# Performance work log

Measured on AMD Instinct MI355X. Metric: run time of the kernel, lower is better.

Reference implementation:

```python
import jax, jax.numpy as jnp
import numpy as np

N_NODES = 10000
DIM = 512
HEADS = 8
HEAD_DIM = DIM // HEADS  # 64
TOPK = 6
EPS = 1e-5
SLOPE = 0.01  # torch LeakyReLU default


def _layernorm(x, w, b):
    mu = x.mean(axis=-1, keepdims=True)
    var = ((x - mu) ** 2).mean(axis=-1, keepdims=True)
    return (x - mu) / jnp.sqrt(var + EPS) * w + b


def setup_inputs() -> dict:
    key = jax.random.key(0)
    ks = jax.random.split(key, 8)

    def w(k, shape):
        return jax.random.normal(k, shape, dtype=jnp.float32) * 0.02

    return {
        "x": jax.random.normal(ks[0], (1, N_NODES, DIM), dtype=jnp.float32),
        "fc1_w": w(ks[1], (DIM, DIM)), "fc1_b": jnp.zeros((DIM,), jnp.float32),
        "wh_w": w(ks[2], (DIM, DIM)), "wh_b": jnp.zeros((DIM,), jnp.float32),
        "wt_w": w(ks[3], (DIM, DIM)), "wt_b": jnp.zeros((DIM,), jnp.float32),
        "q_w": w(ks[4], (DIM, DIM)), "q_b": jnp.zeros((DIM,), jnp.float32),
        "kv_w": w(ks[5], (2 * DIM, DIM)), "kv_b": jnp.zeros((2 * DIM,), jnp.float32),
        "lin_w": w(ks[6], (DIM, DIM)), "lin_b": jnp.zeros((DIM,), jnp.float32),
        "norm_w": jnp.ones((DIM,), jnp.float32),
        "norm_b": jnp.zeros((DIM,), jnp.float32),
    }


def reference(x, fc1_w, fc1_b, wh_w, wh_b, wt_w, wt_b, q_w, q_b,
              kv_w, kv_b, lin_w, lin_b, norm_w, norm_b):
    # x: [1, N, DIM]
    n = x.shape[1]
    scale = HEAD_DIM ** -0.5

    x_input = x
    h = jax.nn.leaky_relu(x @ fc1_w.T + fc1_b, SLOPE)
    h = (h + h.mean(axis=1, keepdims=True)) * 0.5

    e_h = h @ wh_w.T + wh_b            # [1, N, DIM]
    e_t = h @ wt_w.T + wt_b            # [1, N, DIM]

    # dense graph-construction scores + per-row top-k neighbors
    logits = (e_h * scale) @ jnp.swapaxes(e_t, -2, -1)   # [1, N, N]
    _, topk_idx = jax.lax.top_k(logits, TOPK)            # [1, N, TOPK]

    # prototype node = most frequent tail index (torch unique+counts+argsort, top=1)
    counts = jnp.bincount(topk_idx.reshape(-1), length=n)
    top_node = jnp.argmax(counts)

    ins_top = jnp.take(x_input, top_node[None], axis=1)  # [1, 1, DIM]
    q_feat = jnp.take(h, top_node[None], axis=1)[0, 0]   # [DIM]

    # gather k=TOPK neighbor tail embeddings per node
    nb = e_t[0][topk_idx[0]]                              # [N, TOPK, DIM]

    q_heads = (q_feat @ q_w.T + q_b).reshape(HEADS, HEAD_DIM) * scale
    kv = (nb @ kv_w.T + kv_b).reshape(n, TOPK, 2, HEADS, HEAD_DIM)
    k_, v_ = kv[:, :, 0], kv[:, :, 1]                     # [N, TOPK, H, HD]

    attn = jnp.einsum('hd,nehd->nhe', q_heads, k_)        # [N, H, TOPK]
    attn = jax.nn.softmax(attn, axis=-1)
    out = jnp.einsum('nhe,nehd->nhd', attn, v_).reshape(n, DIM)

    e_nh = _layernorm(out, norm_w, norm_b)[None]          # [1, N, DIM]

    s = _layernorm(e_h + e_nh, norm_w, norm_b)
    s = jax.nn.leaky_relu(s @ lin_w.T + lin_b, SLOPE)     # dropout = identity (eval)
    embedding = s + x_input
    return embedding, ins_top
```

## Files before the change

### kernel.cpp

```cpp
#include <hip/hip_runtime.h>
#include <hip/hip_bf16.h>
#include <math.h>

#define N_NODES 10000
#define DIM 512
#define TOPK 6
#define NCHUNK 10
#define CHUNK 1024
#define NL 4
#define NCK 8
#define NC2 16
#define SLOPE 0.01
#define LN_EPS 1e-5f

typedef short bf16x8 __attribute__((ext_vector_type(8)));
typedef float f32x4 __attribute__((ext_vector_type(4)));
typedef double f64x4 __attribute__((ext_vector_type(4)));

__device__ __forceinline__ unsigned pack_key(float v, int idx)
{
    unsigned b = __float_as_uint(v);
    unsigned m = b ^ ((unsigned)((int)b >> 31) | 0x80000000u);
    return (m & 0xFFFFC000u) | (16383u - (unsigned)idx);
}

template <int D>
__device__ __forceinline__ void insert_u(unsigned (&k)[D], unsigned nk)
{
    if (nk > k[D - 1]) {
        k[D - 1] = nk;
#pragma unroll
        for (int s = D - 1; s > 0; s--) {
            unsigned hi = max(k[s], k[s - 1]);
            unsigned lo = min(k[s], k[s - 1]);
            k[s - 1] = hi; k[s] = lo;
        }
    }
}

__device__ __forceinline__ void gload16(const void* g, void* l)
{
    __builtin_amdgcn_global_load_lds(
        (const __attribute__((address_space(1))) void*)g,
        (__attribute__((address_space(3))) void*)l, 16, 0, 0);
}

__global__ __launch_bounds__(256) void colsum_part64(
    const double* __restrict__ h, double* __restrict__ part, int n, int nb)
{
    int b = blockIdx.x;
    int rows_per = (n + nb - 1) / nb;
    int r0 = b * rows_per, r1 = min(n, r0 + rows_per);
    int t = threadIdx.x;
    double s0 = 0.0, s1 = 0.0;
    for (int i = r0; i < r1; i++) {
        s0 += h[(size_t)i * DIM + t];
        s1 += h[(size_t)i * DIM + t + 256];
    }
    part[b * DIM + t] = s0;
    part[b * DIM + t + 256] = s1;
}

__global__ void colmean64(const double* __restrict__ part, double* __restrict__ mean,
                          int nb, int n)
{
    int j = blockIdx.x * blockDim.x + threadIdx.x;
    if (j < DIM) {
        double s = 0.0;
        for (int b = 0; b < nb; b++) s += part[b * DIM + j];
        mean[j] = s / (double)n;
    }
}

__global__ void cast_eh(const double* __restrict__ in, float* __restrict__ of,
                        short* __restrict__ ob)
{
    int i = (blockIdx.x * blockDim.x + threadIdx.x) * 4;
    double2 v0 = *(const double2*)(in + i);
    double2 v1 = *(const double2*)(in + i + 2);
    float4 f = make_float4((float)v0.x, (float)v0.y, (float)v1.x, (float)v1.y);
    *(float4*)(of + i) = f;
    __hip_bfloat16 b0 = __float2bfloat16(f.x), b1 = __float2bfloat16(f.y);
    __hip_bfloat16 b2 = __float2bfloat16(f.z), b3 = __float2bfloat16(f.w);
    short4 s = make_short4(*(short*)&b0, *(short*)&b1, *(short*)&b2, *(short*)&b3);
    *(short4*)(ob + i) = s;
}

__global__ void cast_et(const double* __restrict__ in, short* __restrict__ ob)
{
    int i = (blockIdx.x * blockDim.x + threadIdx.x) * 4;
    double2 v0 = *(const double2*)(in + i);
    double2 v1 = *(const double2*)(in + i + 2);
    __hip_bfloat16 b0 = __float2bfloat16((float)v0.x), b1 = __float2bfloat16((float)v0.y);
    __hip_bfloat16 b2 = __float2bfloat16((float)v1.x), b3 = __float2bfloat16((float)v1.y);
    short4 s = make_short4(*(short*)&b0, *(short*)&b1, *(short*)&b2, *(short*)&b3);
    *(short4*)(ob + i) = s;
}

__global__ void cast_wb(const float* __restrict__ in1, short* __restrict__ o1, int n1,
                        const float* __restrict__ in2, short* __restrict__ o2)
{
    int i = (blockIdx.x * blockDim.x + threadIdx.x) * 4;
    const float* in = (i < n1) ? in1 + i : in2 + (i - n1);
    short* o = (i < n1) ? o1 + i : o2 + (i - n1);
    float4 f = *(const float4*)in;
    __hip_bfloat16 b0 = __float2bfloat16(f.x), b1 = __float2bfloat16(f.y);
    __hip_bfloat16 b2 = __float2bfloat16(f.z), b3 = __float2bfloat16(f.w);
    *(short4*)o = make_short4(*(short*)&b0, *(short*)&b1, *(short*)&b2, *(short*)&b3);
}

template <int POST, bool AF32, bool MIX>
__global__ __launch_bounds__(256, 4) void mfma_gemm_f64(
    const void* __restrict__ Av, const float* __restrict__ W,
    const float* __restrict__ bias, const double* __restrict__ mn,
    double* __restrict__ C, int n, int K, int M)
{
    __shared__ double As[64][18];
    __shared__ double Bs[128][18];
    const int t = threadIdx.x, lane = t & 63, wid = t >> 6;
    const int lx = lane & 15, q = lane >> 4;
    const int wr = (wid >> 1) * 32, wc = (wid & 1) * 64;
    const int i0 = blockIdx.x * 64, j0 = blockIdx.y * 128;

    f64x4 acc[2][4];
#pragma unroll
    for (int a = 0; a < 2; a++)
#pragma unroll
        for (int b = 0; b < 4; b++) acc[a][b] = (f64x4)0.0;

    const int arow = t >> 2, askq = (t & 3) * 4;
    int gi = i0 + arow; if (gi >= n) gi = n - 1;
    const float*  af32 = (const float*)Av + (size_t)gi * K + askq;
    const double* af64 = (const double*)Av + (size_t)gi * K + askq;
    const int brow = t >> 1, bskq = (t & 1) * 8;
    const float* wrow = W + (size_t)(j0 + brow) * K + bskq;

    float4 wv0 = *(const float4*)(wrow);
    float4 wv1 = *(const float4*)(wrow + 4);
    float4 av;
    double2 a0v, a1v;
    if (AF32) av = *(const float4*)(af32);
    else { a0v = *(const double2*)(af64); a1v = *(const double2*)(af64 + 2); }

    for (int k0 = 0; k0 < K; k0 += 16) {
        __syncthreads();
        double m0 = 0, m1 = 0, m2 = 0, m3 = 0;
        if (MIX) {
            double2 mv0 = *(const double2*)(mn + k0 + askq);
            double2 mv1 = *(const double2*)(mn + k0 + askq + 2);
            m0 = mv0.x; m1 = mv0.y; m2 = mv1.x; m3 = mv1.y;
        }
        if (AF32) {
            As[arow][askq]     = (double)av.x; As[arow][askq + 1] = (double)av.y;
            As[arow][askq + 2] = (double)av.z; As[arow][askq + 3] = (double)av.w;
        } else if (MIX) {
            As[arow][askq]     = (a0v.x + m0) * 0.5; As[arow][askq + 1] = (a0v.y + m1) * 0.5;
            As[arow][askq + 2] = (a1v.x + m2) * 0.5; As[arow][askq + 3] = (a1v.y + m3) * 0.5;
        } else {
            As[arow][askq]     = a0v.x; As[arow][askq + 1] = a0v.y;
            As[arow][askq + 2] = a1v.x; As[arow][askq + 3] = a1v.y;
        }
        Bs[brow][bskq]     = (double)wv0.x; Bs[brow][bskq + 1] = (double)wv0.y;
        Bs[brow][bskq + 2] = (double)wv0.z; Bs[brow][bskq + 3] = (double)wv0.w;
        Bs[brow][bskq + 4] = (double)wv1.x; Bs[brow][bskq + 5] = (double)wv1.y;
        Bs[brow][bskq + 6] = (double)wv1.z; Bs[brow][bskq + 7] = (double)wv1.w;
        if (k0 + 16 < K) {
            wv0 = *(const float4*)(wrow + k0 + 16);
            wv1 = *(const float4*)(wrow + k0 + 20);
            if (AF32) av = *(const float4*)(af32 + k0 + 16);
            else { a0v = *(const double2*)(af64 + k0 + 16);
                   a1v = *(const double2*)(af64 + k0 + 18); }
        }
        __syncthreads();

#pragma unroll
        for (int ks = 0; ks < 4; ks++) {
            double a0 = As[wr + lx][ks * 4 + q];
            double a1 = As[wr + 16 + lx][ks * 4 + q];
#pragma unroll
            for (int cf = 0; cf < 4; cf++) {
                double b = Bs[wc + cf * 16 + lx][ks * 4 + q];
                acc[0][cf] = __builtin_amdgcn_mfma_f64_16x16x4f64(a0, b, acc[0][cf], 0, 0, 0);
                acc[1][cf] = __builtin_amdgcn_mfma_f64_16x16x4f64(a1, b, acc[1][cf], 0, 0, 0);
            }
        }
    }

#pragma unroll
    for (int rf = 0; rf < 2; rf++)
#pragma unroll
        for (int cf = 0; cf < 4; cf++)
#pragma unroll
            for (int reg = 0; reg < 4; reg++) {
                int gi2 = i0 + wr + rf * 16 + q * 4 + reg;
                int gj2 = j0 + wc + cf * 16 + lx;
                if (gi2 < n) {
                    double v = acc[rf][cf][reg] + (double)bias[gj2];
                    if (POST == 1) v = (v >= 0.0) ? v : v * SLOPE;
                    C[(size_t)gi2 * M + gj2] = v;
                }
            }
}

__global__ __launch_bounds__(256, 3) void logits_topk_mfma(
    const short* __restrict__ eh, const short* __restrict__ et,
    unsigned* __restrict__ pk, int n)
{
    __shared__ short As[3 * 4096];
    __shared__ short Bs[3 * 4096];
    const int t = threadIdx.x;
    const int lane = t & 63, wid = t >> 6;
    const int lx = lane & 15, q = lane >> 4;

    int id = blockIdx.x, bx, chunk;
    if (id < 632) { chunk = id & 7; bx = id >> 3; }
    else { int r = id - 632; chunk = 8 + (r & 1); bx = r >> 1; }
    const int i0 = bx * 128;
    const int wbase = wid * 32;

    const int jlo = chunk * CHUNK;
    const int jhi = min(n, jlo + CHUNK);
    const int nj = (jhi - jlo + 127) >> 7;
    const int np = nj * 16;

    const int sslot = (t & 3) ^ ((t >> 3) & 3);
    const short* aP[2];
    const short* bP[2];
#pragma unroll
    for (int is = 0; is < 2; is++) {
        int row = is * 64 + (t >> 2);
        int ra = i0 + row; if (ra >= n) ra = n - 1;
        aP[is] = eh + (size_t)ra * DIM + sslot * 8;
    }
    const int slotq = (q ^ ((lx >> 1) & 3)) * 8;
    const int aOff = (wbase + lx) * 32 + slotq;
    const int bOff = lx * 32 + slotq;

    unsigned keys[8][NL];
#pragma unroll
    for (int r = 0; r < 8; r++)
#pragma unroll
        for (int s = 0; s < NL; s++) keys[r][s] = 0u;

    f32x4 acc[2][8];
#pragma unroll
    for (int rf = 0; rf < 2; rf++)
#pragma unroll
        for (int cf = 0; cf < 8; cf++) acc[rf][cf] = (f32x4)0.f;

    auto STAGE = [&](int buf, int ph) {
        int kk = ph & 15;
        if (kk == 0) {
            int j0 = jlo + (ph >> 4) * 128;
#pragma unroll
            for (int is = 0; is < 2; is++) {
                int row = is * 64 + (t >> 2);
                int rb = j0 + row; if (rb >= n) rb = n - 1;
                bP[is] = et + (size_t)rb * DIM + sslot * 8;
            }
        }
        int ko = kk * 32;
#pragma unroll
        for (int is = 0; is < 2; is++) {
            gload16(aP[is] + ko, &As[buf * 4096 + is * 2048 + wid * 512]);
            gload16(bP[is] + ko, &Bs[buf * 4096 + is * 2048 + wid * 512]);
        }
    };

    STAGE(0, 0);
    STAGE(1, 1);
    int cb = 0;
    for (int p = 0; p < np; ++p) {
        __builtin_amdgcn_sched_barrier(0);
        __builtin_amdgcn_s_barrier();
        __builtin_amdgcn_sched_barrier(0);
        if (p + 2 < np) {
            int nb = cb + 2; if (nb >= 3) nb -= 3;
            STAGE(nb, p + 2);
            asm volatile("s_waitcnt vmcnt(8)" ::: "memory");
        } else if (p + 1 < np) {
            asm volatile("s_waitcnt vmcnt(4)" ::: "memory");
        } else {
            asm volatile("s_waitcnt vmcnt(0)" ::: "memory");
        }
        __builtin_amdgcn_sched_barrier(0);
        __builtin_amdgcn_s_barrier();
        __builtin_amdgcn_sched_barrier(0);

        const short* Ab = As + cb * 4096;
        const short* Bb = Bs + cb * 4096;
        bf16x8 a0 = *(const bf16x8*)(Ab + aOff);
        bf16x8 a1 = *(const bf16x8*)(Ab + aOff + 512);
#pragma unroll
        for (int cf = 0; cf < 8; cf++) {
            bf16x8 bw = *(const bf16x8*)(Bb + bOff + cf * 512);
            acc[0][cf] = __builtin_amdgcn_mfma_f32_16x16x32_bf16(
                a0, bw, acc[0][cf], 0, 0, 0);
            acc[1][cf] = __builtin_amdgcn_mfma_f32_16x16x32_bf16(
                a1, bw, acc[1][cf], 0, 0, 0);
        }

        if ((p & 15) == 15) {
            int j0 = jlo + (p >> 4) * 128;
#pragma unroll
            for (int rf = 0; rf < 2; rf++)
#pragma unroll
                for (int cf = 0; cf < 8; cf++) {
                    int gj = j0 + cf * 16 + lx;
                    if (gj < n) {
#pragma unroll
                        for (int reg = 0; reg < 4; reg++)
                            insert_u<NL>(keys[rf * 4 + reg],
                                         pack_key(acc[rf][cf][reg], gj));
                    }
                    acc[rf][cf] = (f32x4)0.f;
                }
        }
        cb = (cb == 2) ? 0 : cb + 1;
    }

#pragma unroll
    for (int rr = 0; rr < 8; rr++) {
        unsigned mk[NCK];
#pragma unroll
        for (int s = 0; s < NL; s++) mk[s] = keys[rr][s];
#pragma unroll
        for (int s = NL; s < NCK; s++) mk[s] = 0u;
        for (int m = 1; m < 16; m <<= 1) {
            unsigned sv[NCK];
#pragma unroll
            for (int s = 0; s < NCK; s++) sv[s] = mk[s];
#pragma unroll
            for (int s = 0; s < NCK; s++) {
                unsigned ov = (unsigned)__shfl_xor((int)sv[s], m);
                insert_u<NCK>(mk, ov);
            }
        }
        if (lx == 0) {
            int rf = rr >> 2, reg = rr & 3;
            int grow = i0 + wbase + rf * 16 + q * 4 + reg;
            if (grow < n) {
#pragma unroll
                for (int s = 0; s < NCK; s++)
                    pk[((size_t)chunk * N_NODES + grow) * NCK + s] = mk[s];
            }
        }
    }
}

template <int POST>
__global__ __launch_bounds__(256, 3) void mfma_gemm_bf16(
    const short* __restrict__ A, const short* __restrict__ W,
    const float* __restrict__ bias, const float* __restrict__ res,
    float* __restrict__ C, int n, int M)
{
    __shared__ short As[2][8192];
    __shared__ short Bs[2][8192];
    const int t = threadIdx.x;
    const int lane = t & 63, wid = t >> 6;
    const int lx = lane & 15, q = lane >> 4;
    const int lx7 = lane & 7;
    const int i0 = blockIdx.x * 128;
    const int j0 = blockIdx.y * 128;
    const int wbase = wid * 32;
    const int srl = lane >> 3;
    const int swz = (lane & 7) ^ srl;

    const short* aP[4];
    const short* bP[4];
#pragma unroll
    for (int is = 0; is < 4; is++) {
        int ra = i0 + is * 32 + wid * 8 + srl; if (ra >= n) ra = n - 1;
        aP[is] = A + (size_t)ra * DIM + swz * 8;
        int rb = j0 + is * 32 + wid * 8 + srl;
        bP[is] = W + (size_t)rb * DIM + swz * 8;
    }
    int aIdx[2], bIdx[2];
#pragma unroll
    for (int ks = 0; ks < 2; ks++) {
        int kap = (ks * 4 + q) ^ lx7;
        aIdx[ks] = (wbase + lx) * 64 + kap * 8;
        bIdx[ks] = lx * 64 + kap * 8;
    }

    f32x4 acc[2][8];
#pragma unroll
    for (int rf = 0; rf < 2; rf++)
#pragma unroll
        for (int cf = 0; cf < 8; cf++) acc[rf][cf] = (f32x4)0.f;

    auto STAGE = [&](int buf, int kk) {
        int ko = kk * 64;
        short* ab = &As[buf][wid * 512];
        short* bb = &Bs[buf][wid * 512];
#pragma unroll
        for (int is = 0; is < 4; is++) {
            gload16(aP[is] + ko, ab + is * 2048);
            gload16(bP[is] + ko, bb + is * 2048);
        }
    };

    STAGE(0, 0);
    for (int p = 0; p < 8; ++p) {
        __builtin_amdgcn_sched_barrier(0);
        __builtin_amdgcn_s_barrier();
        __builtin_amdgcn_sched_barrier(0);
        if (p + 1 < 8) {
            STAGE((p + 1) & 1, p + 1);
            asm volatile("s_waitcnt vmcnt(8)" ::: "memory");
        } else {
            asm volatile("s_waitcnt vmcnt(0)" ::: "memory");
        }
        __builtin_amdgcn_sched_barrier(0);
        __builtin_amdgcn_s_barrier();
        __builtin_amdgcn_sched_barrier(0);

        const short* Ab = As[p & 1];
        const short* Bb = Bs[p & 1];
#pragma unroll
        for (int ks = 0; ks < 2; ks++) {
            bf16x8 a0 = *(const bf16x8*)(Ab + aIdx[ks]);
            bf16x8 a1 = *(const bf16x8*)(Ab + aIdx[ks] + 1024);
#pragma unroll
            for (int cf = 0; cf < 8; cf++) {
                bf16x8 bw = *(const bf16x8*)(Bb + bIdx[ks] + cf * 1024);
                acc[0][cf] = __builtin_amdgcn_mfma_f32_16x16x32_bf16(
                    a0, bw, acc[0][cf], 0, 0, 0);
                acc[1][cf] = __builtin_amdgcn_mfma_f32_16x16x32_bf16(
                    a1, bw, acc[1][cf], 0, 0, 0);
            }
        }
    }

#pragma unroll
    for (int rf = 0; rf < 2; rf++)
#pragma unroll
        for (int cf = 0; cf < 8; cf++)
#pragma unroll
            for (int reg = 0; reg < 4; reg++) {
                int gi = i0 + wbase + rf * 16 + q * 4 + reg;
                int gj = j0 + cf * 16 + lx;
                if (gi < n) {
                    float v = acc[rf][cf][reg] + bias[gj];
                    if (POST >= 1) v = (v >= 0.f) ? v : v * SLOPE;
                    if (POST == 2) v += res[(size_t)gi * M + gj];
                    C[(size_t)gi * M + gj] = v;
                }
            }
}

__global__ void merge_chunks16(const unsigned* __restrict__ pk,
                               int* __restrict__ cand, int n)
{
    int row = blockIdx.x * blockDim.x + threadIdx.x;
    if (row >= n) return;
    unsigned bk[NC2];
#pragma unroll
    for (int s = 0; s < NC2; s++) bk[s] = 0u;
    for (int c = 0; c < NCHUNK; c++) {
#pragma unroll
        for (int s = 0; s < NCK; s++)
            insert_u<NC2>(bk, pk[((size_t)c * n + row) * NCK + s]);
    }
#pragma unroll
    for (int s = 0; s < NC2; s++)
        cand[row * NC2 + s] = 16383 - (int)(bk[s] & 16383u);
}

__global__ __launch_bounds__(64) void refine16(
    const double* __restrict__ ehd, const double* __restrict__ etd,
    const int* __restrict__ cand, int* __restrict__ tki,
    int* __restrict__ counts, int n)
{
    int row = blockIdx.x;
    int lane = threadIdx.x;
    int c = lane >> 2, sub = lane & 3;
    int j = cand[row * NC2 + c];
    const double* er = ehd + (size_t)row * DIM;
    const double* tr = etd + (size_t)j * DIM;
    double s = 0.0;
#pragma unroll 8
    for (int k = sub; k < DIM; k += 4) s += er[k] * tr[k];
    s += __shfl_down(s, 2);
    s += __shfl_down(s, 1);
    double mine = __shfl(s, lane & ~3);
    int rank = 0;
#pragma unroll
    for (int m = 0; m < NC2; m++) {
        double vm = __shfl(s, m * 4);
        int jm = __shfl(j, m * 4);
        bool better = (vm > mine) || (vm == mine && jm < j);
        rank += better ? 1 : 0;
    }
    if (sub == 0 && rank < TOPK) {
        tki[row * TOPK + rank] = j;
        atomicAdd(&counts[j], 1);
    }
}

__global__ __launch_bounds__(1024) void argmax_kernel(
    const int* __restrict__ counts, int n, const float* __restrict__ x,
    int* __restrict__ topn, float* __restrict__ out_ins)
{
    __shared__ unsigned long long red[1024];
    int t = threadIdx.x;
    unsigned long long best = 0;
    for (int j = t; j < n; j += 1024) {
        unsigned long long key =
            ((unsigned long long)(unsigned)counts[j] << 32) | (unsigned)(n - 1 - j);
        if (key > best) best = key;
    }
    red[t] = best;
    __syncthreads();
    for (int s = 512; s > 0; s >>= 1) {
        if (t < s && red[t + s] > red[t]) red[t] = red[t + s];
        __syncthreads();
    }
    int tn = n - 1 - (int)(red[0] & 0xffffffffu);
    if (t == 0) *topn = tn;
    if (t < DIM) out_ins[t] = x[(size_t)tn * DIM + t];
}

__global__ __launch_bounds__(512) void qheads_kernel(
    const double* __restrict__ h2d, const double* __restrict__ mn,
    const int* __restrict__ topn, const float* __restrict__ qw,
    const float* __restrict__ qb, float* __restrict__ qh)
{
    __shared__ float qf[DIM];
    int t = threadIdx.x;
    int tn = *topn;
    qf[t] = (float)((h2d[(size_t)tn * DIM + t] + mn[t]) * 0.5);
    __syncthreads();
    int w = t >> 6, lane = t & 63;
    int jrow = blockIdx.x * 8 + w;
    float s = 0.f;
    for (int k = lane; k < DIM; k += 64) s += qf[k] * qw[(size_t)jrow * DIM + k];
#pragma unroll
    for (int m = 32; m > 0; m >>= 1) s += __shfl_down(s, m);
    if (lane == 0) qh[jrow] = (s + qb[jrow]) * 0.125f;
}

__global__ __launch_bounds__(512) void scores_kernel(
    const float* __restrict__ E, const float* __restrict__ qh, float* __restrict__ sc)
{
    int i = blockIdx.x;
    int t = threadIdx.x, w = t >> 6, lane = t & 63;
    float v = qh[t] * E[(size_t)i * 1024 + t];
#pragma unroll
    for (int m = 32; m > 0; m >>= 1) v += __shfl_down(v, m);
    if (lane == 0) sc[i * 8 + w] = v;
}

__global__ __launch_bounds__(512) void attn_ln_kernel(
    const float* __restrict__ E, const float* __restrict__ sc,
    const int* __restrict__ tki, const float* __restrict__ eh,
    const float* __restrict__ nw, const float* __restrict__ nbias,
    short* __restrict__ sprb, int n)
{
    __shared__ int nb[TOPK];
    __shared__ float red[16];
    __shared__ float stats[2];
    const int i = blockIdx.x;
    const int t = threadIdx.x;
    const int h = t >> 6, lane = t & 63;
    if (t < TOPK) nb[t] = tki[i * TOPK + t];
    __syncthreads();

    float myse = 0.f;
    if (lane < TOPK) myse = sc[(size_t)nb[lane] * 8 + h];
    float se[TOPK];
#pragma unroll
    for (int e = 0; e < TOPK; e++) se[e] = __shfl(myse, e);
    float mx = se[0];
#pragma unroll
    for (int e = 1; e < TOPK; e++) mx = fmaxf(mx, se[e]);
    float wsum = 0.f, w[TOPK];
#pragma unroll
    for (int e = 0; e < TOPK; e++) { w[e] = expf(se[e] - mx); wsum += w[e]; }
    float inv = 1.f / wsum;

    float o = 0.f;
#pragma unroll
    for (int e = 0; e < TOPK; e++) o += w[e] * E[(size_t)nb[e] * 1024 + 512 + t];
    o *= inv;

    float s1 = o, s2 = o * o;
#pragma unroll
    for (int m = 32; m > 0; m >>= 1) { s1 += __shfl_down(s1, m); s2 += __shfl_down(s2, m); }
    if (lane == 0) { red[h] = s1; red[h + 8] = s2; }
    __syncthreads();
    if (t == 0) {
        float a = 0.f, b = 0.f;
#pragma unroll
        for (int k = 0; k < 8; k++) { a += red[k]; b += red[k + 8]; }
        float mu = a * (1.f / 512.f);
        float var = b * (1.f / 512.f) - mu * mu;
        stats[0] = mu; stats[1] = rsqrtf(var + LN_EPS);
    }
    __syncthreads();
    float enh = (o - stats[0]) * stats[1] * nw[t] + nbias[t];
    float t2 = eh[(size_t)i * DIM + t] + enh;
    __syncthreads();

    s1 = t2; s2 = t2 * t2;
#pragma unroll
    for (int m = 32; m > 0; m >>= 1) { s1 += __shfl_down(s1, m); s2 += __shfl_down(s2, m); }
    if (lane == 0) { red[h] = s1; red[h + 8] = s2; }
    __syncthreads();
    if (t == 0) {
        float a = 0.f, b = 0.f;
#pragma unroll
        for (int k = 0; k < 8; k++) { a += red[k]; b += red[k + 8]; }
        float mu = a * (1.f / 512.f);
        float var = b * (1.f / 512.f) - mu * mu;
        stats[0] = mu; stats[1] = rsqrtf(var + LN_EPS);
    }
    __syncthreads();
    float sv = (t2 - stats[0]) * stats[1] * nw[t] + nbias[t];
    __hip_bfloat16 bb = __float2bfloat16(sv);
    sprb[(size_t)i * DIM + t] = *reinterpret_cast<short*>(&bb);
}

extern "C" void kernel_launch(void* const* d_in, const int* in_sizes, int n_in,
                              void* d_out, int out_size, void* d_ws, size_t ws_size,
                              hipStream_t stream)
{
    const float* x     = (const float*)d_in[0];
    const float* fc1_w = (const float*)d_in[1];
    const float* fc1_b = (const float*)d_in[2];
    const float* wh_w  = (const float*)d_in[3];
    const float* wh_b  = (const float*)d_in[4];
    const float* wt_w  = (const float*)d_in[5];
    const float* wt_b  = (const float*)d_in[6];
    const float* q_w   = (const float*)d_in[7];
    const float* q_b   = (const float*)d_in[8];
    const float* kv_w  = (const float*)d_in[9];
    const float* kv_b  = (const float*)d_in[10];
    const float* lin_w = (const float*)d_in[11];
    const float* lin_b = (const float*)d_in[12];
    const float* nw    = (const float*)d_in[13];
    const float* nbias = (const float*)d_in[14];
    float* out = (float*)d_out;

    const int n = N_NODES;
    size_t off = 0;
    auto take = [&](size_t bytes) -> void* {
        void* p = (void*)((char*)d_ws + off);
        off += (bytes + 255) & ~(size_t)255;
        return p;
    };
    double* h2d  = (double*)take((size_t)n * DIM * 8);
    double* ehd  = (double*)take((size_t)n * DIM * 8);
    double* etd  = (double*)take((size_t)n * DIM * 8);
    float*  ehf  = (float*)take((size_t)n * DIM * 4);
    short*  ehb  = (short*)take((size_t)n * DIM * 2);
    short*  etb  = (short*)take((size_t)n * DIM * 2);
    short*  sprb = (short*)take((size_t)n * DIM * 2);
    unsigned* pk = (unsigned*)take((size_t)NCHUNK * n * NCK * 4);
    int*    cand = (int*)take((size_t)n * NC2 * 4);
    int*    tki  = (int*)take((size_t)n * TOPK * 4);
    int*    counts = (int*)take((size_t)n * 4);
    int*    topn = (int*)take(256);
    float*  qh   = (float*)take(DIM * 4);
    float*  sc   = (float*)take((size_t)n * 8 * 4);
    double* part = (double*)take((size_t)160 * DIM * 8);
    double* mean = (double*)take(DIM * 8);
    short*  kvwb = (short*)take((size_t)1024 * DIM * 2);
    short*  linwb = (short*)take((size_t)512 * DIM * 2);
    float* E = (float*)h2d;

    hipMemsetAsync(counts, 0, n * sizeof(int), stream);

    dim3 b256(256);
    const int RB64 = (n + 63) / 64;
    const int RB2  = (n + 127) / 128;

    mfma_gemm_f64<1, true, false><<<dim3(RB64, 4), b256, 0, stream>>>(
        x, fc1_w, fc1_b, nullptr, h2d, n, DIM, DIM);
    colsum_part64<<<dim3(160), b256, 0, stream>>>(h2d, part, n, 160);
    colmean64<<<dim3(2), b256, 0, stream>>>(part, mean, 160, n);
    mfma_gemm_f64<0, false, true><<<dim3(RB64, 4), b256, 0, stream>>>(
        h2d, wh_w, wh_b, mean, ehd, n, DIM, DIM);
    mfma_gemm_f64<0, false, true><<<dim3(RB64, 4), b256, 0, stream>>>(
        h2d, wt_w, wt_b, mean, etd, n, DIM, DIM);
    cast_eh<<<dim3((n * DIM) / 1024), b256, 0, stream>>>(ehd, ehf, ehb);
    cast_et<<<dim3((n * DIM) / 1024), b256, 0, stream>>>(etd, etb);
    cast_wb<<<dim3((1536 * DIM) / 1024), b256, 0, stream>>>(
        kv_w, kvwb, 1024 * DIM, lin_w, linwb);

    logits_topk_mfma<<<dim3(632 + 2 * RB2), b256, 0, stream>>>(ehb, etb, pk, n);
    merge_chunks16<<<dim3((n + 255) / 256), b256, 0, stream>>>(pk, cand, n);
    refine16<<<dim3(n), dim3(64), 0, stream>>>(ehd, etd, cand, tki, counts, n);

    argmax_kernel<<<dim3(1), dim3(1024), 0, stream>>>(counts, n, x, topn,
                                                      out + (size_t)n * DIM);
    qheads_kernel<<<dim3(64), dim3(512), 0, stream>>>(h2d, mean, topn, q_w, q_b, qh);
    mfma_gemm_bf16<0><<<dim3(RB2, 8), b256, 0, stream>>>(
        etb, kvwb, kv_b, nullptr, E, n, 1024);
    scores_kernel<<<dim3(n), dim3(512), 0, stream>>>(E, qh, sc);
    attn_ln_kernel<<<dim3(n), dim3(512), 0, stream>>>(E, sc, tki, ehf, nw, nbias, sprb, n);
    mfma_gemm_bf16<2><<<dim3(RB2, 4), b256, 0, stream>>>(
        sprb, linwb, lin_b, x, out, n, 512);
}
```

Before: 920.3 us.

## Fuse fp32/bf16 casts into f64 GEMM epilogue, double-buffer logits, batch refine rows

The separate cast_eh and cast_et kernels are removed. The f64 GEMM epilogue now writes the float and bf16 copies directly, which avoids re-reading the double outputs. The logits_topk kernel drops from triple to double buffering of shared memory, which cuts LDS use but shortens the prefetch distance. refine16 now packs four rows per 256-thread block instead of one row per 64-thread block.

New measurement: 842.7 us. 8.4% less time.

```diff
diff --git a/kernel.cpp b/kernel.cpp
--- a/kernel.cpp
+++ b/kernel.cpp
@@ -72,31 +72,6 @@
     }
 }
 
-__global__ void cast_eh(const double* __restrict__ in, float* __restrict__ of,
-                        short* __restrict__ ob)
-{
-    int i = (blockIdx.x * blockDim.x + threadIdx.x) * 4;
-    double2 v0 = *(const double2*)(in + i);
-    double2 v1 = *(const double2*)(in + i + 2);
-    float4 f = make_float4((float)v0.x, (float)v0.y, (float)v1.x, (float)v1.y);
-    *(float4*)(of + i) = f;
-    __hip_bfloat16 b0 = __float2bfloat16(f.x), b1 = __float2bfloat16(f.y);
-    __hip_bfloat16 b2 = __float2bfloat16(f.z), b3 = __float2bfloat16(f.w);
-    short4 s = make_short4(*(short*)&b0, *(short*)&b1, *(short*)&b2, *(short*)&b3);
-    *(short4*)(ob + i) = s;
-}
-
-__global__ void cast_et(const double* __restrict__ in, short* __restrict__ ob)
-{
-    int i = (blockIdx.x * blockDim.x + threadIdx.x) * 4;
-    double2 v0 = *(const double2*)(in + i);
-    double2 v1 = *(const double2*)(in + i + 2);
-    __hip_bfloat16 b0 = __float2bfloat16((float)v0.x), b1 = __float2bfloat16((float)v0.y);
-    __hip_bfloat16 b2 = __float2bfloat16((float)v1.x), b3 = __float2bfloat16((float)v1.y);
-    short4 s = make_short4(*(short*)&b0, *(short*)&b1, *(short*)&b2, *(short*)&b3);
-    *(short4*)(ob + i) = s;
-}
-
 __global__ void cast_wb(const float* __restrict__ in1, short* __restrict__ o1, int n1,
                         const float* __restrict__ in2, short* __restrict__ o2)
 {
@@ -109,11 +84,12 @@
     *(short4*)o = make_short4(*(short*)&b0, *(short*)&b1, *(short*)&b2, *(short*)&b3);
 }
 
-template <int POST, bool AF32, bool MIX>
+template <int POST, bool AF32, bool MIX, bool CASTF, bool CASTB>
 __global__ __launch_bounds__(256, 4) void mfma_gemm_f64(
     const void* __restrict__ Av, const float* __restrict__ W,
     const float* __restrict__ bias, const double* __restrict__ mn,
-    double* __restrict__ C, int n, int K, int M)
+    double* __restrict__ C, float* __restrict__ of, short* __restrict__ ob,
+    int n, int K, int M)
 {
     __shared__ double As[64][18];
     __shared__ double Bs[128][18];
@@ -197,7 +173,16 @@
                 if (gi2 < n) {
                     double v = acc[rf][cf][reg] + (double)bias[gj2];
                     if (POST == 1) v = (v >= 0.0) ? v : v * SLOPE;
-                    C[(size_t)gi2 * M + gj2] = v;
+                    size_t idx = (size_t)gi2 * M + gj2;
+                    C[idx] = v;
+                    if (CASTF || CASTB) {
+                        float f = (float)v;
+                        if (CASTF) of[idx] = f;
+                        if (CASTB) {
+                            __hip_bfloat16 bb = __float2bfloat16(f);
+                            ob[idx] = *reinterpret_cast<short*>(&bb);
+                        }
+                    }
                 }
             }
 }
@@ -206,8 +191,8 @@
     const short* __restrict__ eh, const short* __restrict__ et,
     unsigned* __restrict__ pk, int n)
 {
-    __shared__ short As[3 * 4096];
-    __shared__ short Bs[3 * 4096];
+    __shared__ short As[2][4096];
+    __shared__ short Bs[2][4096];
     const int t = threadIdx.x;
     const int lane = t & 63, wid = t >> 6;
     const int lx = lane & 15, q = lane >> 4;
@@ -262,23 +247,18 @@
         int ko = kk * 32;
 #pragma unroll
         for (int is = 0; is < 2; is++) {
-            gload16(aP[is] + ko, &As[buf * 4096 + is * 2048 + wid * 512]);
-            gload16(bP[is] + ko, &Bs[buf * 4096 + is * 2048 + wid * 512]);
+            gload16(aP[is] + ko, &As[buf][is * 2048 + wid * 512]);
+            gload16(bP[is] + ko, &Bs[buf][is * 2048 + wid * 512]);
         }
     };
 
     STAGE(0, 0);
-    STAGE(1, 1);
-    int cb = 0;
     for (int p = 0; p < np; ++p) {
         __builtin_amdgcn_sched_barrier(0);
         __builtin_amdgcn_s_barrier();
         __builtin_amdgcn_sched_barrier(0);
-        if (p + 2 < np) {
-            int nb = cb + 2; if (nb >= 3) nb -= 3;
-            STAGE(nb, p + 2);
-            asm volatile("s_waitcnt vmcnt(8)" ::: "memory");
-        } else if (p + 1 < np) {
+        if (p + 1 < np) {
+            STAGE((p + 1) & 1, p + 1);
             asm volatile("s_waitcnt vmcnt(4)" ::: "memory");
         } else {
             asm volatile("s_waitcnt vmcnt(0)" ::: "memory");
@@ -287,8 +267,8 @@
         __builtin_amdgcn_s_barrier();
         __builtin_amdgcn_sched_barrier(0);
 
-        const short* Ab = As + cb * 4096;
-        const short* Bb = Bs + cb * 4096;
+        const short* Ab = As[p & 1];
+        const short* Bb = Bs[p & 1];
         bf16x8 a0 = *(const bf16x8*)(Ab + aOff);
         bf16x8 a1 = *(const bf16x8*)(Ab + aOff + 512);
 #pragma unroll
@@ -316,7 +296,6 @@
                     acc[rf][cf] = (f32x4)0.f;
                 }
         }
-        cb = (cb == 2) ? 0 : cb + 1;
     }
 
 #pragma unroll
@@ -467,13 +446,14 @@
         cand[row * NC2 + s] = 16383 - (int)(bk[s] & 16383u);
 }
 
-__global__ __launch_bounds__(64) void refine16(
+__global__ __launch_bounds__(256) void refine16(
     const double* __restrict__ ehd, const double* __restrict__ etd,
     const int* __restrict__ cand, int* __restrict__ tki,
     int* __restrict__ counts, int n)
 {
-    int row = blockIdx.x;
-    int lane = threadIdx.x;
+    int row = blockIdx.x * 4 + (threadIdx.x >> 6);
+    if (row >= n) return;
+    int lane = threadIdx.x & 63;
     int c = lane >> 2, sub = lane & 3;
     int j = cand[row * NC2 + c];
     const double* er = ehd + (size_t)row * DIM;
@@ -675,22 +655,20 @@
     const int RB64 = (n + 63) / 64;
     const int RB2  = (n + 127) / 128;
 
-    mfma_gemm_f64<1, true, false><<<dim3(RB64, 4), b256, 0, stream>>>(
-        x, fc1_w, fc1_b, nullptr, h2d, n, DIM, DIM);
+    mfma_gemm_f64<1, true, false, false, false><<<dim3(RB64, 4), b256, 0, stream>>>(
+        x, fc1_w, fc1_b, nullptr, h2d, nullptr, nullptr, n, DIM, DIM);
     colsum_part64<<<dim3(160), b256, 0, stream>>>(h2d, part, n, 160);
     colmean64<<<dim3(2), b256, 0, stream>>>(part, mean, 160, n);
-    mfma_gemm_f64<0, false, true><<<dim3(RB64, 4), b256, 0, stream>>>(
-        h2d, wh_w, wh_b, mean, ehd, n, DIM, DIM);
-    mfma_gemm_f64<0, false, true><<<dim3(RB64, 4), b256, 0, stream>>>(
-        h2d, wt_w, wt_b, mean, etd, n, DIM, DIM);
-    cast_eh<<<dim3((n * DIM) / 1024), b256, 0, stream>>>(ehd, ehf, ehb);
-    cast_et<<<dim3((n * DIM) / 1024), b256, 0, stream>>>(etd, etb);
+    mfma_gemm_f64<0, false, true, true, true><<<dim3(RB64, 4), b256, 0, stream>>>(
+        h2d, wh_w, wh_b, mean, ehd, ehf, ehb, n, DIM, DIM);
+    mfma_gemm_f64<0, false, true, false, true><<<dim3(RB64, 4), b256, 0, stream>>>(
+        h2d, wt_w, wt_b, mean, etd, nullptr, etb, n, DIM, DIM);
     cast_wb<<<dim3((1536 * DIM) / 1024), b256, 0, stream>>>(
         kv_w, kvwb, 1024 * DIM, lin_w, linwb);
 
     logits_topk_mfma<<<dim3(632 + 2 * RB2), b256, 0, stream>>>(ehb, etb, pk, n);
     merge_chunks16<<<dim3((n + 255) / 256), b256, 0, stream>>>(pk, cand, n);
-    refine16<<<dim3(n), dim3(64), 0, stream>>>(ehd, etd, cand, tki, counts, n);
+    refine16<<<dim3((n + 3) / 4), b256, 0, stream>>>(ehd, etd, cand, tki, counts, n);
 
     argmax_kernel<<<dim3(1), dim3(1024), 0, stream>>>(counts, n, x, topn,
                                                       out + (size_t)n * DIM);
```
